# Optimization experiments

Hardware: AMD Instinct MI355X
Metric: run time of the kernel (lower is better)

Reference implementation:

```python
import jax, jax.numpy as jnp
import numpy as np

NEG_SLOPE = 0.1

def leaky(z):
    return jnp.where(z >= 0, z, NEG_SLOPE * z)

def setup_inputs() -> dict:
    key = jax.random.key(0)
    ks = jax.random.split(key, 7)
    N, F = 8192, 256
    s = 1.0 / np.sqrt(F)
    return {
        "x": jax.random.normal(ks[0], (N, F), dtype=jnp.float32),
        "W3": jax.random.normal(ks[1], (1, 2 * F), dtype=jnp.float32) * (1.0 / np.sqrt(2 * F)),
        "b3": jax.random.normal(ks[2], (1,), dtype=jnp.float32) * 0.01,
        "W6": jax.random.normal(ks[3], (F, F), dtype=jnp.float32) * s,
        "b6": jax.random.normal(ks[4], (F,), dtype=jnp.float32) * 0.01,
        "W5": jax.random.normal(ks[5], (F, F), dtype=jnp.float32) * s,
        "b5": jax.random.normal(ks[6], (F,), dtype=jnp.float32) * 0.01,
    }

def reference(x, W3, b3, W6, b6, W5, b5):
    # x: [N, F] node features (original: list of N [1,F] tensors)
    N, F = x.shape
    # g3(concat(n_i, n_j)) == x_i @ Wa + x_j @ Wb + b3, so never build [N,N,2F]
    Wa = W3[0, :F]  # [F]
    Wb = W3[0, F:]  # [F]
    s = x @ Wa      # [N] contribution of n_i
    t = x @ Wb      # [N] contribution of n_j
    W = leaky(s[:, None] + t[None, :] + b3[0])  # [N,N] pairwise weights
    G = leaky(x @ W6.T + b6)                    # [N,F] g6(n_j)
    # sum over j != i of W_ij * G_j, averaged by (N-1)
    diag = leaky(s + t + b3[0])                 # [N] W_ii
    M = (W @ G - diag[:, None] * G) / (N - 1)   # [N,F] aggregated message
    out = leaky(M @ W5.T + b5) + x              # g5(message) + residual
    return out
```

## Files before the change

### kernel.cpp

```cpp
#include <hip/hip_runtime.h>
#include <stdint.h>

#define NR 8192
#define FD 256
#define NCH 1024

typedef __attribute__((ext_vector_type(8))) short bf16x8;
typedef __attribute__((ext_vector_type(4))) float f32x4;

__device__ __forceinline__ float leaky_f(float z){ return z >= 0.0f ? z : 0.1f * z; }

__device__ __forceinline__ unsigned short f2bf(float f){
    union { float f; uint32_t u; } v; v.f = f;
    uint32_t r = v.u + 0x7fffu + ((v.u >> 16) & 1u);
    return (unsigned short)(r >> 16);
}
__device__ __forceinline__ float bf2f(unsigned short h){
    union { uint32_t u; float f; } v; v.u = ((uint32_t)h) << 16;
    return v.f;
}

__global__ __launch_bounds__(256) void ka_prep(
    const float* __restrict__ x,  const float* __restrict__ W3,
    const float* __restrict__ W6, const float* __restrict__ W5,
    float* __restrict__ s, float* __restrict__ t,
    int* __restrict__ rank, int* __restrict__ pos,
    short* __restrict__ xhi, short* __restrict__ xlo,
    short* __restrict__ W6hi, short* __restrict__ W6lo,
    short* __restrict__ W5hi, short* __restrict__ W5lo)
{
    int b = blockIdx.x;
    int tid = threadIdx.x;
    if (b < 512){
        int i = b * 256 + tid;
        bool six = (i < 65536);
        const float* W = six ? W6 : W5;
        short* hi = six ? W6hi : W5hi;
        short* lo = six ? W6lo : W5lo;
        int k = six ? i : i - 65536;
        float v = W[k];
        unsigned short h = f2bf(v);
        hi[k] = (short)h;
        lo[k] = (short)f2bf(v - bf2f(h));
        return;
    }
    int wave = tid >> 6;
    int lane = tid & 63;
    int row  = (b - 512) * 4 + wave;
    const float4* xr = (const float4*)(x + (size_t)row * FD);
    const float4* wa = (const float4*)W3;
    const float4* wb = (const float4*)(W3 + FD);
    float4 xv = xr[lane], av = wa[lane], bv = wb[lane];
    float xe[4] = {xv.x, xv.y, xv.z, xv.w};
    short4 h4, l4;
    short* hp = &h4.x; short* lp = &l4.x;
    #pragma unroll
    for (int e = 0; e < 4; ++e){
        unsigned short h = f2bf(xe[e]);
        hp[e] = (short)h;
        lp[e] = (short)f2bf(xe[e] - bf2f(h));
    }
    *reinterpret_cast<short4*>(xhi + (size_t)row * FD + lane * 4) = h4;
    *reinterpret_cast<short4*>(xlo + (size_t)row * FD + lane * 4) = l4;

    float as = xv.x*av.x + xv.y*av.y + xv.z*av.z + xv.w*av.w;
    float at = xv.x*bv.x + xv.y*bv.y + xv.z*bv.z + xv.w*bv.w;
    #pragma unroll
    for (int off = 32; off > 0; off >>= 1){
        as += __shfl_xor(as, off, 64);
        at += __shfl_xor(at, off, 64);
    }
    if (lane == 0){ s[row] = as; t[row] = at; rank[row] = 0; pos[row] = 0; }
}

__global__ __launch_bounds__(256) void kb_count(const float* __restrict__ t,
                                                const float* __restrict__ s,
                                                const float* __restrict__ b3,
                                                int* __restrict__ rank,
                                                int* __restrict__ pos){
    __shared__ __align__(16) float seg[256];
    int tid = threadIdx.x;
    int j = blockIdx.x * 256 + tid;
    int segBase = blockIdx.y * 256;
    seg[tid] = t[segBase + tid];
    __syncthreads();
    float tj = t[j];
    float theta = -(s[j] + b3[0]);
    int cr = 0, cp = 0;
    #pragma unroll 8
    for (int r = 0; r < 256; r += 4){
        float4 v = *reinterpret_cast<const float4*>(&seg[r]);
        int jp = segBase + r;
        cr += (v.x < tj) || (v.x == tj && (jp + 0) < j);
        cr += (v.y < tj) || (v.y == tj && (jp + 1) < j);
        cr += (v.z < tj) || (v.z == tj && (jp + 2) < j);
        cr += (v.w < tj) || (v.w == tj && (jp + 3) < j);
        cp += (v.x < theta);
        cp += (v.y < theta);
        cp += (v.z < theta);
        cp += (v.w < theta);
    }
    atomicAdd(&rank[j], cr);
    atomicAdd(&pos[j], cp);
}

template<bool SCATTER, bool ADD>
__global__ __launch_bounds__(512, 4) void gemm_nt(
    const short* __restrict__ Ahi, const short* __restrict__ Alo,
    const short* __restrict__ Whi, const short* __restrict__ Wlo,
    const float* __restrict__ bias,
    const float* __restrict__ addend,
    const int* __restrict__ perm,
    const float* __restrict__ tvals,
    float* __restrict__ tsorted,
    float* __restrict__ out)
{
    __shared__ f32x4 red[4][4][64];
    int tid  = threadIdx.x;
    int wave = tid >> 6;
    int lane = tid & 63;
    int rw = wave & 3;
    int kh = wave >> 2;
    int rowBase = blockIdx.y * 64 + rw * 16;
    int colBase = blockIdx.x * 64;

    if (SCATTER && blockIdx.x == 0 && tid < 64){
        int grow = blockIdx.y * 64 + tid;
        tsorted[perm[grow]] = tvals[grow];
    }

    int m16 = lane & 15;
    int k8  = (lane >> 4) * 8;

    f32x4 acc[4];
    #pragma unroll
    for (int c = 0; c < 4; ++c) acc[c] = (f32x4){0.f, 0.f, 0.f, 0.f};

    const short* arh = Ahi + (size_t)(rowBase + m16) * FD + kh * 128 + k8;
    const short* arl = Alo + (size_t)(rowBase + m16) * FD + kh * 128 + k8;

    #pragma unroll
    for (int ks = 0; ks < 4; ++ks){
        int kb = ks * 32;
        bf16x8 ahi = *reinterpret_cast<const bf16x8*>(arh + kb);
        bf16x8 alo = *reinterpret_cast<const bf16x8*>(arl + kb);
        #pragma unroll
        for (int c = 0; c < 4; ++c){
            size_t boff = (size_t)(colBase + c * 16 + m16) * FD + kh * 128 + k8 + kb;
            bf16x8 bhi = *reinterpret_cast<const bf16x8*>(Whi + boff);
            bf16x8 blo = *reinterpret_cast<const bf16x8*>(Wlo + boff);
            acc[c] = __builtin_amdgcn_mfma_f32_16x16x32_bf16(ahi, bhi, acc[c], 0, 0, 0);
            acc[c] = __builtin_amdgcn_mfma_f32_16x16x32_bf16(alo, bhi, acc[c], 0, 0, 0);
            acc[c] = __builtin_amdgcn_mfma_f32_16x16x32_bf16(ahi, blo, acc[c], 0, 0, 0);
        }
    }

    if (kh == 1){
        #pragma unroll
        for (int c = 0; c < 4; ++c) red[rw][c][lane] = acc[c];
    }
    __syncthreads();
    if (kh == 0){
        #pragma unroll
        for (int c = 0; c < 4; ++c){
            f32x4 o = red[rw][c][lane];
            acc[c] = acc[c] + o;
        }
        int rq = (lane >> 4) * 4;
        #pragma unroll
        for (int c = 0; c < 4; ++c){
            int gcol = colBase + c * 16 + m16;
            float bs = bias[gcol];
            #pragma unroll
            for (int j = 0; j < 4; ++j){
                int grow = rowBase + rq + j;
                float v = leaky_f(acc[c][j] + bs);
                if (ADD) v += addend[(size_t)grow * FD + gcol];
                int orow = SCATTER ? perm[grow] : grow;
                out[(size_t)orow * FD + gcol] = v;
            }
        }
    }
}

__global__ __launch_bounds__(256) void kd_partial(const float* __restrict__ Gs,
                                                  const float* __restrict__ ts,
                                                  float* __restrict__ p0,
                                                  float* __restrict__ p1){
    int col = threadIdx.x;
    int chunk = blockIdx.x;
    int base = chunk * 8;
    float s0 = 0.f, s1 = 0.f;
    #pragma unroll
    for (int r = 0; r < 8; ++r){
        float g = Gs[(size_t)(base + r) * FD + col];
        s0 += g;
        s1 += ts[base + r] * g;
    }
    p0[(size_t)chunk * FD + col] = s0;
    p1[(size_t)chunk * FD + col] = s1;
}

__global__ __launch_bounds__(64) void ke_scan(float* __restrict__ p0,
                                              float* __restrict__ p1){
    int bid  = blockIdx.x;
    int lane = threadIdx.x;
    float* p = (bid < 256) ? p0 : p1;
    int col = bid & 255;
    int c0 = lane * 16;
    float v[16];
    #pragma unroll
    for (int k = 0; k < 16; ++k) v[k] = p[(size_t)(c0 + k) * FD + col];
    float run = 0.f;
    #pragma unroll
    for (int k = 0; k < 16; ++k) run += v[k];
    float x = run;
    #pragma unroll
    for (int off = 1; off < 64; off <<= 1){
        float n = __shfl_up(x, off, 64);
        if (lane >= off) x += n;
    }
    float e = x - run;
    #pragma unroll
    for (int k = 0; k < 16; ++k){
        p[(size_t)(c0 + k) * FD + col] = e;
        e += v[k];
    }
    if (lane == 63) p[(size_t)NCH * FD + col] = x;
}

__global__ __launch_bounds__(256) void kf_build(
    const float* __restrict__ s, const float* __restrict__ t,
    const float* __restrict__ b3,
    const int* __restrict__ rank, const int* __restrict__ pos,
    const float* __restrict__ ts, const float* __restrict__ Gs,
    const float* __restrict__ p0, const float* __restrict__ p1,
    short* __restrict__ Mhi, short* __restrict__ Mlo)
{
    int col = threadIdx.x;
    int i0 = blockIdx.x * 4;
    float T0 = p0[(size_t)NCH * FD + col];
    float T1 = p1[(size_t)NCH * FD + col];
    float c = b3[0];
    const float inv = 1.0f / (float)(NR - 1);
    #pragma unroll
    for (int r = 0; r < 4; ++r){
        int i = i0 + r;
        float sic = s[i] + c;
        float diag = leaky_f(sic + t[i]);
        int ps = pos[i];
        int rk = rank[i];
        int ch = ps >> 3;
        float P0 = p0[(size_t)ch * FD + col];
        float P1 = p1[(size_t)ch * FD + col];
        for (int r2 = ch * 8; r2 < ps; ++r2){
            float g2 = Gs[(size_t)r2 * FD + col];
            P0 += g2;
            P1 += ts[r2] * g2;
        }
        float g = Gs[(size_t)rk * FD + col];
        float full = sic * T0 + T1;
        float act  = sic * (T0 - P0) + (T1 - P1);
        float m = (0.1f * full + 0.9f * act - diag * g) * inv;
        unsigned short h = f2bf(m);
        Mhi[(size_t)i * FD + col] = (short)h;
        Mlo[(size_t)i * FD + col] = (short)f2bf(m - bf2f(h));
    }
}

extern "C" void kernel_launch(void* const* d_in, const int* in_sizes, int n_in,
                              void* d_out, int out_size, void* d_ws, size_t ws_size,
                              hipStream_t stream)
{
    const float* x  = (const float*)d_in[0];
    const float* W3 = (const float*)d_in[1];
    const float* b3 = (const float*)d_in[2];
    const float* W6 = (const float*)d_in[3];
    const float* b6 = (const float*)d_in[4];
    const float* W5 = (const float*)d_in[5];
    const float* b5 = (const float*)d_in[6];
    float* out = (float*)d_out;

    char* ws = (char*)d_ws;
    size_t off = 0;
    auto alloc = [&](size_t bytes) -> void* {
        void* p = ws + off;
        off += (bytes + 255) & ~(size_t)255;
        return p;
    };
    float*  s    = (float*)alloc(NR * 4);
    float*  t    = (float*)alloc(NR * 4);
    float*  ts   = (float*)alloc(NR * 4);
    int*    rank = (int*)  alloc(NR * 4);
    int*    pos  = (int*)  alloc(NR * 4);
    float*  p0   = (float*)alloc((size_t)(NCH + 1) * FD * 4);
    float*  p1   = (float*)alloc((size_t)(NCH + 1) * FD * 4);
    short*  W6hi = (short*)alloc(FD * FD * 2);
    short*  W6lo = (short*)alloc(FD * FD * 2);
    short*  W5hi = (short*)alloc(FD * FD * 2);
    short*  W5lo = (short*)alloc(FD * FD * 2);
    short*  xhi  = (short*)alloc((size_t)NR * FD * 2);
    short*  xlo  = (short*)alloc((size_t)NR * FD * 2);
    short*  Mhi  = (short*)alloc((size_t)NR * FD * 2);
    short*  Mlo  = (short*)alloc((size_t)NR * FD * 2);
    float*  Gs   = (float*)alloc((size_t)NR * FD * 4);
    (void)ws_size; (void)in_sizes; (void)n_in; (void)out_size;

    ka_prep<<<dim3(512 + NR / 4), dim3(256), 0, stream>>>(
        x, W3, W6, W5, s, t, rank, pos, xhi, xlo, W6hi, W6lo, W5hi, W5lo);
    kb_count<<<dim3(32, 32), dim3(256), 0, stream>>>(t, s, b3, rank, pos);
    gemm_nt<true, false><<<dim3(FD / 64, NR / 64), dim3(512), 0, stream>>>(
        xhi, xlo, W6hi, W6lo, b6, nullptr, rank, t, ts, Gs);
    kd_partial<<<dim3(NCH), dim3(256), 0, stream>>>(Gs, ts, p0, p1);
    ke_scan<<<dim3(512), dim3(64), 0, stream>>>(p0, p1);
    kf_build<<<dim3(NR / 4), dim3(256), 0, stream>>>(
        s, t, b3, rank, pos, ts, Gs, p0, p1, Mhi, Mlo);
    gemm_nt<false, true><<<dim3(FD / 64, NR / 64), dim3(512), 0, stream>>>(
        Mhi, Mlo, W5hi, W5lo, b5, x, nullptr, nullptr, nullptr, out);
}
```

Baseline: 158.3 us.

## Fuse all seven stages into one cooperative persistent kernel with grid syncs

```diff
diff --git a/kernel.cpp b/kernel.cpp
--- a/kernel.cpp
+++ b/kernel.cpp
@@ -1,4 +1,5 @@
 #include <hip/hip_runtime.h>
+#include <hip/hip_cooperative_groups.h>
 #include <stdint.h>
 
 #define NR 8192
@@ -7,6 +8,8 @@
 
 typedef __attribute__((ext_vector_type(8))) short bf16x8;
 typedef __attribute__((ext_vector_type(4))) float f32x4;
+
+namespace cg = cooperative_groups;
 
 __device__ __forceinline__ float leaky_f(float z){ return z >= 0.0f ? z : 0.1f * z; }
 
@@ -20,7 +23,8 @@
     return v.f;
 }
 
-__global__ __launch_bounds__(256) void ka_prep(
+
+__device__ __forceinline__ void phaseA(int b, int tid,
     const float* __restrict__ x,  const float* __restrict__ W3,
     const float* __restrict__ W6, const float* __restrict__ W5,
     float* __restrict__ s, float* __restrict__ t,
@@ -29,66 +33,66 @@
     short* __restrict__ W6hi, short* __restrict__ W6lo,
     short* __restrict__ W5hi, short* __restrict__ W5lo)
 {
-    int b = blockIdx.x;
-    int tid = threadIdx.x;
-    if (b < 512){
-        int i = b * 256 + tid;
-        bool six = (i < 65536);
+    int gt = b * 256 + tid;
+    {
+        bool six = gt < FD * FD;
         const float* W = six ? W6 : W5;
         short* hi = six ? W6hi : W5hi;
         short* lo = six ? W6lo : W5lo;
-        int k = six ? i : i - 65536;
+        int k = six ? gt : gt - FD * FD;
         float v = W[k];
         unsigned short h = f2bf(v);
         hi[k] = (short)h;
         lo[k] = (short)f2bf(v - bf2f(h));
-        return;
-    }
-    int wave = tid >> 6;
-    int lane = tid & 63;
-    int row  = (b - 512) * 4 + wave;
-    const float4* xr = (const float4*)(x + (size_t)row * FD);
+    }
+    if (gt < NR){ rank[gt] = 0; pos[gt] = 0; }
+    int wave = tid >> 6, lane = tid & 63;
+    int w = b * 4 + wave;
     const float4* wa = (const float4*)W3;
     const float4* wb = (const float4*)(W3 + FD);
-    float4 xv = xr[lane], av = wa[lane], bv = wb[lane];
-    float xe[4] = {xv.x, xv.y, xv.z, xv.w};
-    short4 h4, l4;
-    short* hp = &h4.x; short* lp = &l4.x;
-    #pragma unroll
-    for (int e = 0; e < 4; ++e){
-        unsigned short h = f2bf(xe[e]);
-        hp[e] = (short)h;
-        lp[e] = (short)f2bf(xe[e] - bf2f(h));
-    }
-    *reinterpret_cast<short4*>(xhi + (size_t)row * FD + lane * 4) = h4;
-    *reinterpret_cast<short4*>(xlo + (size_t)row * FD + lane * 4) = l4;
-
-    float as = xv.x*av.x + xv.y*av.y + xv.z*av.z + xv.w*av.w;
-    float at = xv.x*bv.x + xv.y*bv.y + xv.z*bv.z + xv.w*bv.w;
-    #pragma unroll
-    for (int off = 32; off > 0; off >>= 1){
-        as += __shfl_xor(as, off, 64);
-        at += __shfl_xor(at, off, 64);
-    }
-    if (lane == 0){ s[row] = as; t[row] = at; rank[row] = 0; pos[row] = 0; }
-}
-
-__global__ __launch_bounds__(256) void kb_count(const float* __restrict__ t,
-                                                const float* __restrict__ s,
-                                                const float* __restrict__ b3,
-                                                int* __restrict__ rank,
-                                                int* __restrict__ pos){
-    __shared__ __align__(16) float seg[256];
-    int tid = threadIdx.x;
-    int j = blockIdx.x * 256 + tid;
-    int segBase = blockIdx.y * 256;
-    seg[tid] = t[segBase + tid];
+    float4 av = wa[lane], bv = wb[lane];
+    #pragma unroll
+    for (int rr = 0; rr < 4; ++rr){
+        int row = w * 4 + rr;
+        float4 xv = ((const float4*)(x + (size_t)row * FD))[lane];
+        float xe[4] = {xv.x, xv.y, xv.z, xv.w};
+        short4 h4, l4;
+        short* hp = &h4.x; short* lp = &l4.x;
+        #pragma unroll
+        for (int e = 0; e < 4; ++e){
+            unsigned short h = f2bf(xe[e]);
+            hp[e] = (short)h;
+            lp[e] = (short)f2bf(xe[e] - bf2f(h));
+        }
+        *reinterpret_cast<short4*>(xhi + (size_t)row * FD + lane * 4) = h4;
+        *reinterpret_cast<short4*>(xlo + (size_t)row * FD + lane * 4) = l4;
+        float as = xv.x*av.x + xv.y*av.y + xv.z*av.z + xv.w*av.w;
+        float at = xv.x*bv.x + xv.y*bv.y + xv.z*bv.z + xv.w*bv.w;
+        #pragma unroll
+        for (int off = 32; off > 0; off >>= 1){
+            as += __shfl_xor(as, off, 64);
+            at += __shfl_xor(at, off, 64);
+        }
+        if (lane == 0){ s[row] = as; t[row] = at; }
+    }
+}
+
+__device__ __forceinline__ void phaseB(int b, int tid,
+    const float* __restrict__ t, const float* __restrict__ s,
+    const float* __restrict__ b3,
+    int* __restrict__ rank, int* __restrict__ pos)
+{
+    __shared__ __align__(16) float seg[512];
+    int j = (b >> 4) * 256 + tid;
+    int segBase = (b & 15) * 512;
+    seg[tid]       = t[segBase + tid];
+    seg[tid + 256] = t[segBase + tid + 256];
     __syncthreads();
     float tj = t[j];
     float theta = -(s[j] + b3[0]);
     int cr = 0, cp = 0;
     #pragma unroll 8
-    for (int r = 0; r < 256; r += 4){
+    for (int r = 0; r < 512; r += 4){
         float4 v = *reinterpret_cast<const float4*>(&seg[r]);
         int jp = segBase + r;
         cr += (v.x < tj) || (v.x == tj && (jp + 0) < j);
@@ -105,48 +109,39 @@
 }
 
 template<bool SCATTER, bool ADD>
-__global__ __launch_bounds__(512, 4) void gemm_nt(
+__device__ __forceinline__ void gemm_phase(int b, int tid,
     const short* __restrict__ Ahi, const short* __restrict__ Alo,
     const short* __restrict__ Whi, const short* __restrict__ Wlo,
-    const float* __restrict__ bias,
-    const float* __restrict__ addend,
-    const int* __restrict__ perm,
-    const float* __restrict__ tvals,
-    float* __restrict__ tsorted,
-    float* __restrict__ out)
-{
-    __shared__ f32x4 red[4][4][64];
-    int tid  = threadIdx.x;
-    int wave = tid >> 6;
-    int lane = tid & 63;
-    int rw = wave & 3;
-    int kh = wave >> 2;
-    int rowBase = blockIdx.y * 64 + rw * 16;
-    int colBase = blockIdx.x * 64;
-
-    if (SCATTER && blockIdx.x == 0 && tid < 64){
-        int grow = blockIdx.y * 64 + tid;
-        tsorted[perm[grow]] = tvals[grow];
-    }
-
-    int m16 = lane & 15;
-    int k8  = (lane >> 4) * 8;
-
+    const float* __restrict__ bias, const float* __restrict__ addend,
+    const int* __restrict__ perm, const float* __restrict__ tvals,
+    float* __restrict__ tsorted, float* __restrict__ out)
+{
+    int wave = tid >> 6, lane = tid & 63;
+    int tileRow = b >> 2;
+    int rowBase = tileRow * 64 + wave * 16;
+    int colBase = (b & 3) * 64;
+
+    if (SCATTER && (b & 3) == 0 && tid < 64){
+        int row = tileRow * 64 + tid;
+        tsorted[perm[row]] = tvals[row];
+    }
+
+    int m16 = lane & 15, k8 = (lane >> 4) * 8;
     f32x4 acc[4];
     #pragma unroll
     for (int c = 0; c < 4; ++c) acc[c] = (f32x4){0.f, 0.f, 0.f, 0.f};
 
-    const short* arh = Ahi + (size_t)(rowBase + m16) * FD + kh * 128 + k8;
-    const short* arl = Alo + (size_t)(rowBase + m16) * FD + kh * 128 + k8;
-
-    #pragma unroll
-    for (int ks = 0; ks < 4; ++ks){
+    const short* arh = Ahi + (size_t)(rowBase + m16) * FD + k8;
+    const short* arl = Alo + (size_t)(rowBase + m16) * FD + k8;
+
+    #pragma unroll
+    for (int ks = 0; ks < 8; ++ks){
         int kb = ks * 32;
         bf16x8 ahi = *reinterpret_cast<const bf16x8*>(arh + kb);
         bf16x8 alo = *reinterpret_cast<const bf16x8*>(arl + kb);
         #pragma unroll
         for (int c = 0; c < 4; ++c){
-            size_t boff = (size_t)(colBase + c * 16 + m16) * FD + kh * 128 + k8 + kb;
+            size_t boff = (size_t)(colBase + c * 16 + m16) * FD + k8 + kb;
             bf16x8 bhi = *reinterpret_cast<const bf16x8*>(Whi + boff);
             bf16x8 blo = *reinterpret_cast<const bf16x8*>(Wlo + boff);
             acc[c] = __builtin_amdgcn_mfma_f32_16x16x32_bf16(ahi, bhi, acc[c], 0, 0, 0);
@@ -155,58 +150,50 @@
         }
     }
 
-    if (kh == 1){
-        #pragma unroll
-        for (int c = 0; c < 4; ++c) red[rw][c][lane] = acc[c];
-    }
-    __syncthreads();
-    if (kh == 0){
-        #pragma unroll
-        for (int c = 0; c < 4; ++c){
-            f32x4 o = red[rw][c][lane];
-            acc[c] = acc[c] + o;
-        }
-        int rq = (lane >> 4) * 4;
-        #pragma unroll
-        for (int c = 0; c < 4; ++c){
-            int gcol = colBase + c * 16 + m16;
-            float bs = bias[gcol];
-            #pragma unroll
-            for (int j = 0; j < 4; ++j){
-                int grow = rowBase + rq + j;
-                float v = leaky_f(acc[c][j] + bs);
-                if (ADD) v += addend[(size_t)grow * FD + gcol];
-                int orow = SCATTER ? perm[grow] : grow;
-                out[(size_t)orow * FD + gcol] = v;
-            }
-        }
-    }
-}
-
-__global__ __launch_bounds__(256) void kd_partial(const float* __restrict__ Gs,
-                                                  const float* __restrict__ ts,
-                                                  float* __restrict__ p0,
-                                                  float* __restrict__ p1){
-    int col = threadIdx.x;
-    int chunk = blockIdx.x;
-    int base = chunk * 8;
-    float s0 = 0.f, s1 = 0.f;
-    #pragma unroll
-    for (int r = 0; r < 8; ++r){
-        float g = Gs[(size_t)(base + r) * FD + col];
-        s0 += g;
-        s1 += ts[base + r] * g;
-    }
-    p0[(size_t)chunk * FD + col] = s0;
-    p1[(size_t)chunk * FD + col] = s1;
-}
-
-__global__ __launch_bounds__(64) void ke_scan(float* __restrict__ p0,
-                                              float* __restrict__ p1){
-    int bid  = blockIdx.x;
-    int lane = threadIdx.x;
-    float* p = (bid < 256) ? p0 : p1;
-    int col = bid & 255;
+    int rq = (lane >> 4) * 4;
+    #pragma unroll
+    for (int c = 0; c < 4; ++c){
+        int gcol = colBase + c * 16 + m16;
+        float bs = bias[gcol];
+        #pragma unroll
+        for (int j = 0; j < 4; ++j){
+            int grow = rowBase + rq + j;
+            float v = leaky_f(acc[c][j] + bs);
+            if (ADD) v += addend[(size_t)grow * FD + gcol];
+            int orow = SCATTER ? perm[grow] : grow;
+            out[(size_t)orow * FD + gcol] = v;
+        }
+    }
+}
+
+__device__ __forceinline__ void phaseD(int b, int tid,
+    const float* __restrict__ Gs, const float* __restrict__ ts,
+    float* __restrict__ p0, float* __restrict__ p1)
+{
+    int col = tid;
+    #pragma unroll
+    for (int c2 = 0; c2 < 2; ++c2){
+        int chunk = b * 2 + c2;
+        int base = chunk * 8;
+        float s0 = 0.f, s1 = 0.f;
+        #pragma unroll
+        for (int r = 0; r < 8; ++r){
+            float g = Gs[(size_t)(base + r) * FD + col];
+            s0 += g;
+            s1 += ts[base + r] * g;
+        }
+        p0[(size_t)chunk * FD + col] = s0;
+        p1[(size_t)chunk * FD + col] = s1;
+    }
+}
+
+__device__ __forceinline__ void phaseE(int b, int tid,
+    float* __restrict__ p0, float* __restrict__ p1)
+{
+    int wave = tid >> 6, lane = tid & 63;
+    int w = b * 4 + wave;
+    float* p = (w < 256) ? p0 : p1;
+    int col = w & 255;
     int c0 = lane * 16;
     float v[16];
     #pragma unroll
@@ -214,22 +201,22 @@
     float run = 0.f;
     #pragma unroll
     for (int k = 0; k < 16; ++k) run += v[k];
-    float x = run;
+    float xx = run;
     #pragma unroll
     for (int off = 1; off < 64; off <<= 1){
-        float n = __shfl_up(x, off, 64);
-        if (lane >= off) x += n;
-    }
-    float e = x - run;
+        float n = __shfl_up(xx, off, 64);
+        if (lane >= off) xx += n;
+    }
+    float e = xx - run;
     #pragma unroll
     for (int k = 0; k < 16; ++k){
         p[(size_t)(c0 + k) * FD + col] = e;
         e += v[k];
     }
-    if (lane == 63) p[(size_t)NCH * FD + col] = x;
-}
-
-__global__ __launch_bounds__(256) void kf_build(
+    if (lane == 63) p[(size_t)NCH * FD + col] = xx;
+}
+
+__device__ __forceinline__ void phaseF(int b, int tid,
     const float* __restrict__ s, const float* __restrict__ t,
     const float* __restrict__ b3,
     const int* __restrict__ rank, const int* __restrict__ pos,
@@ -237,14 +224,13 @@
     const float* __restrict__ p0, const float* __restrict__ p1,
     short* __restrict__ Mhi, short* __restrict__ Mlo)
 {
-    int col = threadIdx.x;
-    int i0 = blockIdx.x * 4;
+    int col = tid;
+    int i0 = b * 16;
     float T0 = p0[(size_t)NCH * FD + col];
     float T1 = p1[(size_t)NCH * FD + col];
     float c = b3[0];
     const float inv = 1.0f / (float)(NR - 1);
-    #pragma unroll
-    for (int r = 0; r < 4; ++r){
+    for (int r = 0; r < 16; ++r){
         int i = i0 + r;
         float sic = s[i] + c;
         float diag = leaky_f(sic + t[i]);
@@ -266,6 +252,75 @@
         Mhi[(size_t)i * FD + col] = (short)h;
         Mlo[(size_t)i * FD + col] = (short)f2bf(m - bf2f(h));
     }
+}
+
+__global__ __launch_bounds__(256, 2) void mega(
+    const float* __restrict__ x,  const float* __restrict__ W3,
+    const float* __restrict__ b3, const float* __restrict__ W6,
+    const float* __restrict__ b6, const float* __restrict__ W5,
+    const float* __restrict__ b5, float* __restrict__ out,
+    float* __restrict__ s, float* __restrict__ t, float* __restrict__ ts,
+    int* __restrict__ rank, int* __restrict__ pos,
+    float* __restrict__ p0, float* __restrict__ p1,
+    short* __restrict__ W6hi, short* __restrict__ W6lo,
+    short* __restrict__ W5hi, short* __restrict__ W5lo,
+    short* __restrict__ xhi, short* __restrict__ xlo,
+    short* __restrict__ Mhi, short* __restrict__ Mlo,
+    float* __restrict__ Gs)
+{
+    cg::grid_group grid = cg::this_grid();
+    int b = blockIdx.x, tid = threadIdx.x;
+
+    phaseA(b, tid, x, W3, W6, W5, s, t, rank, pos, xhi, xlo,
+           W6hi, W6lo, W5hi, W5lo);
+    grid.sync();
+    phaseB(b, tid, t, s, b3, rank, pos);
+    grid.sync();
+    gemm_phase<true, false>(b, tid, xhi, xlo, W6hi, W6lo, b6, nullptr,
+                            rank, t, ts, Gs);
+    grid.sync();
+    phaseD(b, tid, Gs, ts, p0, p1);
+    grid.sync();
+    if (b < 128) phaseE(b, tid, p0, p1);
+    grid.sync();
+    phaseF(b, tid, s, t, b3, rank, pos, ts, Gs, p0, p1, Mhi, Mlo);
+    grid.sync();
+    gemm_phase<false, true>(b, tid, Mhi, Mlo, W5hi, W5lo, b5, x,
+                            nullptr, nullptr, nullptr, out);
+}
+
+__global__ __launch_bounds__(256) void kA(
+    const float* x, const float* W3, const float* W6, const float* W5,
+    float* s, float* t, int* rank, int* pos, short* xhi, short* xlo,
+    short* W6hi, short* W6lo, short* W5hi, short* W5lo){
+    phaseA(blockIdx.x, threadIdx.x, x, W3, W6, W5, s, t, rank, pos,
+           xhi, xlo, W6hi, W6lo, W5hi, W5lo);
+}
+__global__ __launch_bounds__(256) void kB(
+    const float* t, const float* s, const float* b3, int* rank, int* pos){
+    phaseB(blockIdx.x, threadIdx.x, t, s, b3, rank, pos);
+}
+template<bool SCATTER, bool ADD>
+__global__ __launch_bounds__(256) void kGemm(
+    const short* Ahi, const short* Alo, const short* Whi, const short* Wlo,
+    const float* bias, const float* addend, const int* perm,
+    const float* tvals, float* tsorted, float* out){
+    gemm_phase<SCATTER, ADD>(blockIdx.x, threadIdx.x, Ahi, Alo, Whi, Wlo,
+                             bias, addend, perm, tvals, tsorted, out);
+}
+__global__ __launch_bounds__(256) void kD(
+    const float* Gs, const float* ts, float* p0, float* p1){
+    phaseD(blockIdx.x, threadIdx.x, Gs, ts, p0, p1);
+}
+__global__ __launch_bounds__(256) void kE(float* p0, float* p1){
+    phaseE(blockIdx.x, threadIdx.x, p0, p1);
+}
+__global__ __launch_bounds__(256) void kF(
+    const float* s, const float* t, const float* b3, const int* rank,
+    const int* pos, const float* ts, const float* Gs,
+    const float* p0, const float* p1, short* Mhi, short* Mlo){
+    phaseF(blockIdx.x, threadIdx.x, s, t, b3, rank, pos, ts, Gs, p0, p1,
+           Mhi, Mlo);
 }
 
 extern "C" void kernel_launch(void* const* d_in, const int* in_sizes, int n_in,
@@ -306,15 +361,28 @@
     float*  Gs   = (float*)alloc((size_t)NR * FD * 4);
     (void)ws_size; (void)in_sizes; (void)n_in; (void)out_size;
 
-    ka_prep<<<dim3(512 + NR / 4), dim3(256), 0, stream>>>(
-        x, W3, W6, W5, s, t, rank, pos, xhi, xlo, W6hi, W6lo, W5hi, W5lo);
-    kb_count<<<dim3(32, 32), dim3(256), 0, stream>>>(t, s, b3, rank, pos);
-    gemm_nt<true, false><<<dim3(FD / 64, NR / 64), dim3(512), 0, stream>>>(
-        xhi, xlo, W6hi, W6lo, b6, nullptr, rank, t, ts, Gs);
-    kd_partial<<<dim3(NCH), dim3(256), 0, stream>>>(Gs, ts, p0, p1);
-    ke_scan<<<dim3(512), dim3(64), 0, stream>>>(p0, p1);
-    kf_build<<<dim3(NR / 4), dim3(256), 0, stream>>>(
-        s, t, b3, rank, pos, ts, Gs, p0, p1, Mhi, Mlo);
-    gemm_nt<false, true><<<dim3(FD / 64, NR / 64), dim3(512), 0, stream>>>(
-        Mhi, Mlo, W5hi, W5lo, b5, x, nullptr, nullptr, nullptr, out);
-}
+    void* args[] = {
+        (void*)&x, (void*)&W3, (void*)&b3, (void*)&W6, (void*)&b6,
+        (void*)&W5, (void*)&b5, (void*)&out,
+        (void*)&s, (void*)&t, (void*)&ts, (void*)&rank, (void*)&pos,
+        (void*)&p0, (void*)&p1,
+        (void*)&W6hi, (void*)&W6lo, (void*)&W5hi, (void*)&W5lo,
+        (void*)&xhi, (void*)&xlo, (void*)&Mhi, (void*)&Mlo, (void*)&Gs
+    };
+    hipError_t e = hipLaunchCooperativeKernel((const void*)mega, dim3(512),
+                                              dim3(256), args, 0, stream);
+    if (e != hipSuccess){
+        (void)hipGetLastError();
+        kA<<<dim3(512), dim3(256), 0, stream>>>(
+            x, W3, W6, W5, s, t, rank, pos, xhi, xlo, W6hi, W6lo, W5hi, W5lo);
+        kB<<<dim3(512), dim3(256), 0, stream>>>(t, s, b3, rank, pos);
+        kGemm<true, false><<<dim3(512), dim3(256), 0, stream>>>(
+            xhi, xlo, W6hi, W6lo, b6, nullptr, rank, t, ts, Gs);
+        kD<<<dim3(512), dim3(256), 0, stream>>>(Gs, ts, p0, p1);
+        kE<<<dim3(128), dim3(256), 0, stream>>>(p0, p1);
+        kF<<<dim3(512), dim3(256), 0, stream>>>(
+            s, t, b3, rank, pos, ts, Gs, p0, p1, Mhi, Mlo);
+        kGemm<false, true><<<dim3(512), dim3(256), 0, stream>>>(
+            Mhi, Mlo, W5hi, W5lo, b5, x, nullptr, nullptr, nullptr, out);
+    }
+}
```

Result: slower. 516.1 us (+226.0%).

## Retile split-bf16 GEMM to 32x64 blocks with full-K per wave, no reduction

Applied to the files above, without the earlier changes.

```diff
diff --git a/kernel.cpp b/kernel.cpp
--- a/kernel.cpp
+++ b/kernel.cpp
@@ -20,7 +20,7 @@
     return v.f;
 }
 
-__global__ __launch_bounds__(256) void ka_prep(
+__global__ __launch_bounds__(256) void kA(
     const float* __restrict__ x,  const float* __restrict__ W3,
     const float* __restrict__ W6, const float* __restrict__ W5,
     float* __restrict__ s, float* __restrict__ t,
@@ -29,28 +29,26 @@
     short* __restrict__ W6hi, short* __restrict__ W6lo,
     short* __restrict__ W5hi, short* __restrict__ W5lo)
 {
-    int b = blockIdx.x;
-    int tid = threadIdx.x;
+    int b = blockIdx.x, tid = threadIdx.x;
     if (b < 512){
         int i = b * 256 + tid;
-        bool six = (i < 65536);
+        bool six = i < FD * FD;
         const float* W = six ? W6 : W5;
         short* hi = six ? W6hi : W5hi;
         short* lo = six ? W6lo : W5lo;
-        int k = six ? i : i - 65536;
+        int k = six ? i : i - FD * FD;
         float v = W[k];
         unsigned short h = f2bf(v);
         hi[k] = (short)h;
         lo[k] = (short)f2bf(v - bf2f(h));
         return;
     }
-    int wave = tid >> 6;
-    int lane = tid & 63;
-    int row  = (b - 512) * 4 + wave;
-    const float4* xr = (const float4*)(x + (size_t)row * FD);
+    int wave = tid >> 6, lane = tid & 63;
+    int row = (b - 512) * 4 + wave;
     const float4* wa = (const float4*)W3;
     const float4* wb = (const float4*)(W3 + FD);
-    float4 xv = xr[lane], av = wa[lane], bv = wb[lane];
+    float4 av = wa[lane], bv = wb[lane];
+    float4 xv = ((const float4*)(x + (size_t)row * FD))[lane];
     float xe[4] = {xv.x, xv.y, xv.z, xv.w};
     short4 h4, l4;
     short* hp = &h4.x; short* lp = &l4.x;
@@ -62,7 +60,6 @@
     }
     *reinterpret_cast<short4*>(xhi + (size_t)row * FD + lane * 4) = h4;
     *reinterpret_cast<short4*>(xlo + (size_t)row * FD + lane * 4) = l4;
-
     float as = xv.x*av.x + xv.y*av.y + xv.z*av.z + xv.w*av.w;
     float at = xv.x*bv.x + xv.y*bv.y + xv.z*bv.z + xv.w*bv.w;
     #pragma unroll
@@ -73,11 +70,11 @@
     if (lane == 0){ s[row] = as; t[row] = at; rank[row] = 0; pos[row] = 0; }
 }
 
-__global__ __launch_bounds__(256) void kb_count(const float* __restrict__ t,
-                                                const float* __restrict__ s,
-                                                const float* __restrict__ b3,
-                                                int* __restrict__ rank,
-                                                int* __restrict__ pos){
+__global__ __launch_bounds__(256) void kB(
+    const float* __restrict__ t, const float* __restrict__ s,
+    const float* __restrict__ b3,
+    int* __restrict__ rank, int* __restrict__ pos)
+{
     __shared__ __align__(16) float seg[256];
     int tid = threadIdx.x;
     int j = blockIdx.x * 256 + tid;
@@ -105,48 +102,40 @@
 }
 
 template<bool SCATTER, bool ADD>
-__global__ __launch_bounds__(512, 4) void gemm_nt(
+__global__ __launch_bounds__(256) void kGemm(
     const short* __restrict__ Ahi, const short* __restrict__ Alo,
     const short* __restrict__ Whi, const short* __restrict__ Wlo,
-    const float* __restrict__ bias,
-    const float* __restrict__ addend,
-    const int* __restrict__ perm,
-    const float* __restrict__ tvals,
-    float* __restrict__ tsorted,
-    float* __restrict__ out)
-{
-    __shared__ f32x4 red[4][4][64];
-    int tid  = threadIdx.x;
-    int wave = tid >> 6;
-    int lane = tid & 63;
-    int rw = wave & 3;
-    int kh = wave >> 2;
-    int rowBase = blockIdx.y * 64 + rw * 16;
-    int colBase = blockIdx.x * 64;
-
-    if (SCATTER && blockIdx.x == 0 && tid < 64){
-        int grow = blockIdx.y * 64 + tid;
-        tsorted[perm[grow]] = tvals[grow];
-    }
-
-    int m16 = lane & 15;
-    int k8  = (lane >> 4) * 8;
-
-    f32x4 acc[4];
-    #pragma unroll
-    for (int c = 0; c < 4; ++c) acc[c] = (f32x4){0.f, 0.f, 0.f, 0.f};
-
-    const short* arh = Ahi + (size_t)(rowBase + m16) * FD + kh * 128 + k8;
-    const short* arl = Alo + (size_t)(rowBase + m16) * FD + kh * 128 + k8;
-
-    #pragma unroll
-    for (int ks = 0; ks < 4; ++ks){
+    const float* __restrict__ bias, const float* __restrict__ addend,
+    const int* __restrict__ perm, const float* __restrict__ tvals,
+    float* __restrict__ tsorted, float* __restrict__ out)
+{
+    int b = blockIdx.x, tid = threadIdx.x;
+    int wave = tid >> 6, lane = tid & 63;
+    int tileRow = b >> 2;
+    int rowBase = tileRow * 32 + (wave & 1) * 16;
+    int colBase = (b & 3) * 64 + (wave >> 1) * 32;
+
+    if (SCATTER && (b & 3) == 0 && tid < 32){
+        int row = tileRow * 32 + tid;
+        tsorted[perm[row]] = tvals[row];
+    }
+
+    int m16 = lane & 15, k8 = (lane >> 4) * 8;
+    f32x4 acc[2];
+    acc[0] = (f32x4){0.f, 0.f, 0.f, 0.f};
+    acc[1] = (f32x4){0.f, 0.f, 0.f, 0.f};
+
+    const short* arh = Ahi + (size_t)(rowBase + m16) * FD + k8;
+    const short* arl = Alo + (size_t)(rowBase + m16) * FD + k8;
+
+    #pragma unroll
+    for (int ks = 0; ks < 8; ++ks){
         int kb = ks * 32;
         bf16x8 ahi = *reinterpret_cast<const bf16x8*>(arh + kb);
         bf16x8 alo = *reinterpret_cast<const bf16x8*>(arl + kb);
         #pragma unroll
-        for (int c = 0; c < 4; ++c){
-            size_t boff = (size_t)(colBase + c * 16 + m16) * FD + kh * 128 + k8 + kb;
+        for (int c = 0; c < 2; ++c){
+            size_t boff = (size_t)(colBase + c * 16 + m16) * FD + k8 + kb;
             bf16x8 bhi = *reinterpret_cast<const bf16x8*>(Whi + boff);
             bf16x8 blo = *reinterpret_cast<const bf16x8*>(Wlo + boff);
             acc[c] = __builtin_amdgcn_mfma_f32_16x16x32_bf16(ahi, bhi, acc[c], 0, 0, 0);
@@ -155,38 +144,26 @@
         }
     }
 
-    if (kh == 1){
+    int rq = (lane >> 4) * 4;
+    #pragma unroll
+    for (int c = 0; c < 2; ++c){
+        int gcol = colBase + c * 16 + m16;
+        float bs = bias[gcol];
         #pragma unroll
-        for (int c = 0; c < 4; ++c) red[rw][c][lane] = acc[c];
-    }
-    __syncthreads();
-    if (kh == 0){
-        #pragma unroll
-        for (int c = 0; c < 4; ++c){
-            f32x4 o = red[rw][c][lane];
-            acc[c] = acc[c] + o;
+        for (int j = 0; j < 4; ++j){
+            int grow = rowBase + rq + j;
+            float v = leaky_f(acc[c][j] + bs);
+            if (ADD) v += addend[(size_t)grow * FD + gcol];
+            int orow = SCATTER ? perm[grow] : grow;
+            out[(size_t)orow * FD + gcol] = v;
         }
-        int rq = (lane >> 4) * 4;
-        #pragma unroll
-        for (int c = 0; c < 4; ++c){
-            int gcol = colBase + c * 16 + m16;
-            float bs = bias[gcol];
-            #pragma unroll
-            for (int j = 0; j < 4; ++j){
-                int grow = rowBase + rq + j;
-                float v = leaky_f(acc[c][j] + bs);
-                if (ADD) v += addend[(size_t)grow * FD + gcol];
-                int orow = SCATTER ? perm[grow] : grow;
-                out[(size_t)orow * FD + gcol] = v;
-            }
-        }
-    }
-}
-
-__global__ __launch_bounds__(256) void kd_partial(const float* __restrict__ Gs,
-                                                  const float* __restrict__ ts,
-                                                  float* __restrict__ p0,
-                                                  float* __restrict__ p1){
+    }
+}
+
+__global__ __launch_bounds__(256) void kD(
+    const float* __restrict__ Gs, const float* __restrict__ ts,
+    float* __restrict__ p0, float* __restrict__ p1)
+{
     int col = threadIdx.x;
     int chunk = blockIdx.x;
     int base = chunk * 8;
@@ -201,9 +178,10 @@
     p1[(size_t)chunk * FD + col] = s1;
 }
 
-__global__ __launch_bounds__(64) void ke_scan(float* __restrict__ p0,
-                                              float* __restrict__ p1){
-    int bid  = blockIdx.x;
+__global__ __launch_bounds__(64) void kE(float* __restrict__ p0,
+                                         float* __restrict__ p1)
+{
+    int bid = blockIdx.x;
     int lane = threadIdx.x;
     float* p = (bid < 256) ? p0 : p1;
     int col = bid & 255;
@@ -214,22 +192,22 @@
     float run = 0.f;
     #pragma unroll
     for (int k = 0; k < 16; ++k) run += v[k];
-    float x = run;
+    float xx = run;
     #pragma unroll
     for (int off = 1; off < 64; off <<= 1){
-        float n = __shfl_up(x, off, 64);
-        if (lane >= off) x += n;
-    }
-    float e = x - run;
+        float n = __shfl_up(xx, off, 64);
+        if (lane >= off) xx += n;
+    }
+    float e = xx - run;
     #pragma unroll
     for (int k = 0; k < 16; ++k){
         p[(size_t)(c0 + k) * FD + col] = e;
         e += v[k];
     }
-    if (lane == 63) p[(size_t)NCH * FD + col] = x;
-}
-
-__global__ __launch_bounds__(256) void kf_build(
+    if (lane == 63) p[(size_t)NCH * FD + col] = xx;
+}
+
+__global__ __launch_bounds__(256) void kF(
     const float* __restrict__ s, const float* __restrict__ t,
     const float* __restrict__ b3,
     const int* __restrict__ rank, const int* __restrict__ pos,
@@ -306,15 +284,15 @@
     float*  Gs   = (float*)alloc((size_t)NR * FD * 4);
     (void)ws_size; (void)in_sizes; (void)n_in; (void)out_size;
 
-    ka_prep<<<dim3(512 + NR / 4), dim3(256), 0, stream>>>(
+    kA<<<dim3(512 + NR / 4), dim3(256), 0, stream>>>(
         x, W3, W6, W5, s, t, rank, pos, xhi, xlo, W6hi, W6lo, W5hi, W5lo);
-    kb_count<<<dim3(32, 32), dim3(256), 0, stream>>>(t, s, b3, rank, pos);
-    gemm_nt<true, false><<<dim3(FD / 64, NR / 64), dim3(512), 0, stream>>>(
+    kB<<<dim3(32, 32), dim3(256), 0, stream>>>(t, s, b3, rank, pos);
+    kGemm<true, false><<<dim3(1024), dim3(256), 0, stream>>>(
         xhi, xlo, W6hi, W6lo, b6, nullptr, rank, t, ts, Gs);
-    kd_partial<<<dim3(NCH), dim3(256), 0, stream>>>(Gs, ts, p0, p1);
-    ke_scan<<<dim3(512), dim3(64), 0, stream>>>(p0, p1);
-    kf_build<<<dim3(NR / 4), dim3(256), 0, stream>>>(
+    kD<<<dim3(NCH), dim3(256), 0, stream>>>(Gs, ts, p0, p1);
+    kE<<<dim3(512), dim3(64), 0, stream>>>(p0, p1);
+    kF<<<dim3(NR / 4), dim3(256), 0, stream>>>(
         s, t, b3, rank, pos, ts, Gs, p0, p1, Mhi, Mlo);
-    gemm_nt<false, true><<<dim3(FD / 64, NR / 64), dim3(512), 0, stream>>>(
+    kGemm<false, true><<<dim3(1024), dim3(256), 0, stream>>>(
         Mhi, Mlo, W5hi, W5lo, b5, x, nullptr, nullptr, nullptr, out);
 }
```

Result: slower. 162.6 us (+2.7%).
